# Optimization experiments

Hardware: AMD Instinct MI355X
Metric: run time of the kernel (lower is better)

## Reference

```python
import jax, jax.numpy as jnp
import numpy as np

N_ING, N_TASTE, D, E = 50000, 20000, 128, 600000


def setup_inputs() -> dict:
    key = jax.random.key(0)
    ks = jax.random.split(key, 13)
    s = 1.0 / np.sqrt(D)
    src = jax.random.randint(ks[2], (E,), 0, N_ING)
    dst = jax.random.randint(ks[3], (E,), 0, N_TASTE)
    return {
        "x_ing": jax.random.normal(ks[0], (N_ING, D), jnp.float32),
        "x_taste": jax.random.normal(ks[1], (N_TASTE, D), jnp.float32),
        "edge_index": jnp.stack([src, dst]),  # [2, E], row0=src(ingredient), row1=dst(taste)
        "W_ing": (jax.random.normal(ks[4], (D, D), jnp.float32) * s),
        "b_ing": jnp.zeros((D,), jnp.float32),
        "W_taste": (jax.random.normal(ks[5], (D, D), jnp.float32) * s),
        "b_taste": jnp.zeros((D,), jnp.float32),
        "a_src": (jax.random.normal(ks[6], (D,), jnp.float32) * s),
        "a_dst": (jax.random.normal(ks[7], (D,), jnp.float32) * s),
        "Wk": (jax.random.normal(ks[8], (D, D), jnp.float32) * s),
        "bk": jnp.zeros((D,), jnp.float32),
        "q": (jax.random.normal(ks[9], (D,), jnp.float32) * s),
    }


def reference(x_ing, x_taste, edge_index, W_ing, b_ing, W_taste, b_taste,
              a_src, a_dst, Wk, bk, q):
    # Input DictDropout(0.4) treated as identity (eval mode) for determinism.
    Nt = x_taste.shape[0]
    src, dst = edge_index[0], edge_index[1]

    # Per-node-type projections (HANConv.proj), heads=1 so head dim == D
    h_src = x_ing @ W_ing + b_ing      # [Ni, D]
    h_dst = x_taste @ W_taste + b_taste  # [Nt, D]

    # GAT-style additive attention logits
    al_src = h_src @ a_src  # [Ni]
    al_dst = h_dst @ a_dst  # [Nt]
    alpha = jax.nn.leaky_relu(al_src[src] + al_dst[dst], negative_slope=0.2)  # [E]

    # scatter-softmax over destination nodes
    amax = jax.ops.segment_max(alpha, dst, num_segments=Nt)        # [Nt]
    e = jnp.exp(alpha - amax[dst])                                  # [E]
    denom = jax.ops.segment_sum(e, dst, num_segments=Nt)           # [Nt]
    attn = e / jnp.maximum(denom[dst], 1e-16)                       # [E]

    # weighted scatter-add aggregation + ReLU (as in HANConv per edge type)
    msgs = h_src[src] * attn[:, None]                               # [E, D]
    out = jax.ops.segment_sum(msgs, dst, num_segments=Nt)          # [Nt, D]
    out = jax.nn.relu(out)

    # semantic attention across relation types (single relation -> beta == 1)
    score = jnp.sum(jnp.tanh(out @ Wk + bk).mean(axis=0) * q)       # scalar
    beta = jax.nn.softmax(score[None])[0]
    out = beta * out

    # TasteGNN applies GELU (torch default: exact erf form)
    return jax.nn.gelu(out, approximate=False)
```

## Files before the change

### kernel.cpp

```cpp
#include <hip/hip_runtime.h>
#include <hip/hip_bf16.h>

#define D 128
#define HB 288

using bf16x8 = __attribute__((ext_vector_type(8))) short;
using f32x4  = __attribute__((ext_vector_type(4))) float;

__device__ __forceinline__ ushort bf16bits(float f) {
    return __hip_bfloat16_raw(__float2bfloat16(f)).x;
}
__device__ __forceinline__ uint pack2(float lo, float hi) {
    return ((uint)bf16bits(hi) << 16) | (uint)bf16bits(lo);
}

__global__ __launch_bounds__(256)
void prep_kernel(const float* __restrict__ W_ing, const float* __restrict__ b_ing,
                 const float* __restrict__ W_taste, const float* __restrict__ b_taste,
                 const float* __restrict__ a_src, const float* __restrict__ a_dst,
                 ushort* __restrict__ Wt, float* __restrict__ v, float* __restrict__ consts,
                 int* __restrict__ count, int* __restrict__ total, int nt) {
    int t = threadIdx.x, b = blockIdx.x;
    if (b == 0) {
        __shared__ float red[D];
        int k = t;
        if (k < D) {
            float sv = 0.f;
            for (int d2 = 0; d2 < D; ++d2) sv += W_taste[k * D + d2] * a_dst[d2];
            v[k] = sv;
            red[k] = b_ing[k] * a_src[k];
        }
        __syncthreads();
        for (int s = 64; s > 0; s >>= 1) { if (k < s) red[k] += red[k + s]; __syncthreads(); }
        if (k == 0) consts[0] = red[0];
        __syncthreads();
        if (k < D) red[k] = b_taste[k] * a_dst[k];
        __syncthreads();
        for (int s = 64; s > 0; s >>= 1) { if (k < s) red[k] += red[k + s]; __syncthreads(); }
        if (k == 0) consts[1] = red[0];
    } else if (b <= 2) {
        int base = (b - 1) * 8192 + t * 32;
        #pragma unroll 8
        for (int i = 0; i < 32; ++i) {
            int idx = base + i;
            int n = idx >> 7, k = idx & 127;
            Wt[n * D + k] = bf16bits(W_ing[k * D + n]);
        }
    } else {
        int gid = (b - 3) * 256 + t;
        if (gid < nt) count[gid] = 0;
        if (gid == nt) *total = 0;
    }
}

__global__ __launch_bounds__(256)
void front_kernel(const float* __restrict__ x, const ushort* __restrict__ Wt,
                  const float* __restrict__ b, const float* __restrict__ avec,
                  const float* __restrict__ consts,
                  ushort* __restrict__ h16, float* __restrict__ al, int nrows, int GB,
                  const float* __restrict__ x_taste, const float* __restrict__ v,
                  int nt, float* __restrict__ al_dst,
                  const int* __restrict__ dstv, int E, int* __restrict__ count,
                  int* __restrict__ rank) {
    __shared__ __align__(16) ushort Xs[128 * 64];
    __shared__ __align__(16) ushort Ws[128 * 64];
    int t = threadIdx.x;

    if (blockIdx.x >= GB) {
        int rb = blockIdx.x - GB;
        if (rb < 512) {
            int lane = t & 63;
            int wave = rb * 4 + (t >> 6);
            float2 uv = ((const float2*)v)[lane];
            float c = consts[1];
            for (int r = wave; r < nt; r += 2048) {
                float2 xv = ((const float2*)(x_taste + (size_t)r * D))[lane];
                float p = xv.x * uv.x + xv.y * uv.y;
                #pragma unroll
                for (int off = 32; off; off >>= 1) p += __shfl_xor(p, off, 64);
                if (lane == 0) al_dst[r] = p + c;
            }
        } else {
            int tbase = (rb - 512) * 256 + t;
            int stride = HB * 256;
            for (int i0 = tbase; i0 < E; i0 += stride * 8) {
                int dv[8], idx[8], rv[8];
                #pragma unroll
                for (int k = 0; k < 8; ++k) {
                    idx[k] = i0 + k * stride;
                    dv[k] = (idx[k] < E) ? dstv[idx[k]] : -1;
                }
                #pragma unroll
                for (int k = 0; k < 8; ++k)
                    rv[k] = (dv[k] >= 0) ? atomicAdd(&count[dv[k]], 1) : 0;
                #pragma unroll
                for (int k = 0; k < 8; ++k)
                    if (dv[k] >= 0) rank[idx[k]] = rv[k];
            }
        }
        return;
    }

    int row0 = blockIdx.x * 128;
    int l = t & 63, w = t >> 6;
    int lr = l & 15, lq = l >> 4;
    f32x4 acc[2][8];
    #pragma unroll
    for (int i = 0; i < 2; ++i)
        #pragma unroll
        for (int j = 0; j < 8; ++j) acc[i][j] = f32x4{0.f, 0.f, 0.f, 0.f};

    int rowA0 = w * 32 + lr;
    int rowA1 = rowA0 + 16;
    int sw = lr & 7;
    int r = t >> 1;
    int kh = (t & 1) * 32;
    bool valid = (row0 + r) < nrows;

    #pragma unroll
    for (int h = 0; h < 2; ++h) {
        int k0 = h * 64;
        {
            const float* xp = x + (size_t)(row0 + r) * D + k0 + kh;
            const ushort* wp = Wt + (size_t)r * D + k0 + kh;
            int base_us = r * 64;
            #pragma unroll
            for (int j = 0; j < 4; ++j) {
                int c16 = (kh >> 3) + j;
                int off = base_us + ((c16 ^ (r & 7)) << 3);
                float4 a = valid ? *(const float4*)(xp + j * 8)     : make_float4(0.f, 0.f, 0.f, 0.f);
                float4 c = valid ? *(const float4*)(xp + j * 8 + 4) : make_float4(0.f, 0.f, 0.f, 0.f);
                uint4 pk;
                pk.x = pack2(a.x, a.y); pk.y = pack2(a.z, a.w);
                pk.z = pack2(c.x, c.y); pk.w = pack2(c.z, c.w);
                *(uint4*)&Xs[off] = pk;
                *(uint4*)&Ws[off] = *(const uint4*)(wp + j * 8);
            }
        }
        __syncthreads();
        #pragma unroll
        for (int s = 0; s < 2; ++s) {
            int c16 = s * 4 + lq;
            bf16x8 A0 = *(const bf16x8*)&Xs[rowA0 * 64 + ((c16 ^ sw) << 3)];
            bf16x8 A1 = *(const bf16x8*)&Xs[rowA1 * 64 + ((c16 ^ sw) << 3)];
            #pragma unroll
            for (int ct = 0; ct < 8; ++ct) {
                int rn = ct * 16 + lr;
                bf16x8 B = *(const bf16x8*)&Ws[rn * 64 + ((c16 ^ sw) << 3)];
                acc[0][ct] = __builtin_amdgcn_mfma_f32_16x16x32_bf16(A0, B, acc[0][ct], 0, 0, 0);
                acc[1][ct] = __builtin_amdgcn_mfma_f32_16x16x32_bf16(A1, B, acc[1][ct], 0, 0, 0);
            }
        }
        __syncthreads();
    }

    float bv[8], av[8];
    #pragma unroll
    for (int ct = 0; ct < 8; ++ct) { bv[ct] = b[ct * 16 + lr]; av[ct] = avec[ct * 16 + lr]; }
    float c0 = consts[0];
    #pragma unroll
    for (int rt = 0; rt < 2; ++rt) {
        #pragma unroll
        for (int rr = 0; rr < 4; ++rr) {
            int gr = row0 + w * 32 + rt * 16 + lq * 4 + rr;
            float p = 0.f;
            ushort hrow[8];
            #pragma unroll
            for (int ct = 0; ct < 8; ++ct) {
                float hv = acc[rt][ct][rr] + bv[ct];
                p = fmaf(hv, av[ct], p);
                hrow[ct] = bf16bits(hv);
            }
            p += __shfl_xor(p, 1, 64); p += __shfl_xor(p, 2, 64);
            p += __shfl_xor(p, 4, 64); p += __shfl_xor(p, 8, 64);
            if (gr < nrows) {
                #pragma unroll
                for (int ct = 0; ct < 8; ++ct)
                    h16[(size_t)gr * D + ct * 16 + lr] = hrow[ct];
                if (lr == 0) al[gr] = p + c0;
            }
        }
    }
}

__global__ __launch_bounds__(256)
void alloc_kernel(const int* __restrict__ count, int n, int* __restrict__ offs,
                  int* __restrict__ total) {
    int gid = blockIdx.x * blockDim.x + threadIdx.x;
    int lane = threadIdx.x & 63;
    int v = (gid < n) ? count[gid] : 0;
    int s = v;
    #pragma unroll
    for (int off = 1; off < 64; off <<= 1) {
        int t2 = __shfl_up(s, off, 64);
        if (lane >= off) s += t2;
    }
    int wavesum = __shfl(s, 63, 64);
    int base = 0;
    if (lane == 63) base = atomicAdd(total, wavesum);
    base = __shfl(base, 63, 64);
    if (gid < n) offs[gid] = base + s - v;
}

__global__ __launch_bounds__(256)
void scatter_kernel(const int* __restrict__ srcv, const int* __restrict__ dstv,
                    const int* __restrict__ rank, int E,
                    const int* __restrict__ offs, uint* __restrict__ es) {
    int tbase = blockIdx.x * blockDim.x + threadIdx.x;
    int stride = gridDim.x * blockDim.x;
    for (int i0 = tbase; i0 < E; i0 += stride * 4) {
        int idx[4], sv[4], dv[4], rv[4], ov[4];
        #pragma unroll
        for (int k = 0; k < 4; ++k) {
            idx[k] = i0 + k * stride;
            bool val = idx[k] < E;
            sv[k] = val ? srcv[idx[k]] : 0;
            dv[k] = val ? dstv[idx[k]] : 0;
            rv[k] = val ? rank[idx[k]] : 0;
        }
        #pragma unroll
        for (int k = 0; k < 4; ++k) ov[k] = offs[dv[k]];
        #pragma unroll
        for (int k = 0; k < 4; ++k)
            if (idx[k] < E) es[ov[k] + rv[k]] = (uint)sv[k];
    }
}

__global__ __launch_bounds__(256)
void agg_kernel(const ushort* __restrict__ h16, const int* __restrict__ offs,
                const int* __restrict__ count, const uint* __restrict__ es,
                const float* __restrict__ al_src, const float* __restrict__ al_dst,
                int nt, float* __restrict__ outp) {
    int lane = threadIdx.x & 63;
    int n = blockIdx.x * (blockDim.x >> 6) + (threadIdx.x >> 6);
    if (n >= nt) return;
    int beg = offs[n], cnt = count[n];
    float acc0 = 0.f, acc1 = 0.f;
    if (cnt > 0) {
        float ald = al_dst[n];
        uint s0 = 0, s1 = 0;
        float a0 = -1e30f, a1 = -1e30f;
        if (lane < cnt) {
            s0 = es[beg + lane];
            float t = al_src[s0] + ald; a0 = t > 0.f ? t : 0.2f * t;
        }
        if (64 + lane < cnt) {
            s1 = es[beg + 64 + lane];
            float t = al_src[s1] + ald; a1 = t > 0.f ? t : 0.2f * t;
        }
        float m = fmaxf(a0, a1);
        for (int i = 128 + lane; i < cnt; i += 64) {
            uint s = es[beg + i];
            float t = al_src[s] + ald; t = t > 0.f ? t : 0.2f * t;
            m = fmaxf(m, t);
        }
        #pragma unroll
        for (int off = 32; off; off >>= 1) m = fmaxf(m, __shfl_xor(m, off, 64));

        float w0 = (lane < cnt) ? __expf(a0 - m) : 0.f;
        float w1 = (64 + lane < cnt) ? __expf(a1 - m) : 0.f;
        float ssum = w0 + w1;
        for (int i = 128 + lane; i < cnt; i += 64) {
            uint s = es[beg + i];
            float t = al_src[s] + ald; t = t > 0.f ? t : 0.2f * t;
            ssum += __expf(t - m);
        }
        #pragma unroll
        for (int off = 32; off; off >>= 1) ssum += __shfl_xor(ssum, off, 64);
        float inv = 1.f / fmaxf(ssum, 1e-16f);

        for (int base = 0; base < cnt; base += 64) {
            uint pkl;
            if (base == 0)       pkl = (s0 << 16) | ((__float_as_uint(w0) + 0x8000u) >> 16);
            else if (base == 64) pkl = (s1 << 16) | ((__float_as_uint(w1) + 0x8000u) >> 16);
            else {
                pkl = 0;
                if (base + lane < cnt) {
                    uint s = es[beg + base + lane];
                    float t = al_src[s] + ald; t = t > 0.f ? t : 0.2f * t;
                    float wv = __expf(t - m);
                    pkl = (s << 16) | ((__float_as_uint(wv) + 0x8000u) >> 16);
                }
            }
            if (base + lane >= cnt) pkl = 0;
            int k = cnt - base; if (k > 64) k = 64;
            int kpad = (k + 7) & ~7;
            for (int i = 0; i < kpad; i += 8) {
                uint pk[8], hv[8];
                #pragma unroll
                for (int j = 0; j < 8; ++j) pk[j] = __shfl(pkl, i + j, 64);
                #pragma unroll
                for (int j = 0; j < 8; ++j) {
                    uint s2 = pk[j] >> 16;
                    hv[j] = ((const uint*)(h16 + (size_t)s2 * D))[lane];
                }
                #pragma unroll
                for (int j = 0; j < 8; ++j) {
                    float w  = __uint_as_float(pk[j] << 16);
                    float lo = __uint_as_float((hv[j] & 0xffffu) << 16);
                    float hi = __uint_as_float(hv[j] & 0xffff0000u);
                    acc0 = fmaf(w, lo, acc0);
                    acc1 = fmaf(w, hi, acc1);
                }
            }
        }
        acc0 *= inv; acc1 *= inv;
    }
    float o0 = acc0 > 0.f ? acc0 : 0.f;
    float o1 = acc1 > 0.f ? acc1 : 0.f;
    o0 = 0.5f * o0 * (1.f + erff(o0 * 0.70710678118654752f));
    o1 = 0.5f * o1 * (1.f + erff(o1 * 0.70710678118654752f));
    *(float2*)(outp + (size_t)n * D + 2 * lane) = make_float2(o0, o1);
}

extern "C" void kernel_launch(void* const* d_in, const int* in_sizes, int n_in,
                              void* d_out, int out_size, void* d_ws, size_t ws_size,
                              hipStream_t stream) {
    const float* x_ing   = (const float*)d_in[0];
    const float* x_taste = (const float*)d_in[1];
    const int*   edge    = (const int*)d_in[2];
    const float* W_ing   = (const float*)d_in[3];
    const float* b_ing   = (const float*)d_in[4];
    const float* W_taste = (const float*)d_in[5];
    const float* b_taste = (const float*)d_in[6];
    const float* a_src   = (const float*)d_in[7];
    const float* a_dst   = (const float*)d_in[8];
    float* outp = (float*)d_out;

    int Ni = in_sizes[0] / D;
    int Nt = in_sizes[1] / D;
    int E  = in_sizes[2] / 2;
    const int* srcv = edge;
    const int* dstv = edge + E;

    char* ws = (char*)d_ws;
    size_t off = 0;
    auto alloc = [&](size_t bytes) { void* p = ws + off; off += (bytes + 255) & ~(size_t)255; return p; };
    ushort* h16   = (ushort*)alloc((size_t)Ni * D * 2);
    ushort* Wt    = (ushort*)alloc((size_t)D * D * 2);
    float* v      = (float*)alloc(D * 4);
    float* consts = (float*)alloc(2 * 4);
    float* al_src = (float*)alloc((size_t)Ni * 4);
    float* al_dst = (float*)alloc((size_t)Nt * 4);
    int* count    = (int*)alloc((size_t)Nt * 4);
    int* offs     = (int*)alloc((size_t)Nt * 4);
    int* rank     = (int*)alloc((size_t)E * 4);
    int* total    = (int*)alloc(4);
    uint* es      = (uint*)alloc((size_t)E * 4);

    int GB = (Ni + 127) / 128;
    int zb = (Nt + 1 + 255) / 256;
    prep_kernel<<<3 + zb, 256, 0, stream>>>(W_ing, b_ing, W_taste, b_taste, a_src, a_dst,
                                            Wt, v, consts, count, total, Nt);
    front_kernel<<<GB + 512 + HB, 256, 0, stream>>>(x_ing, Wt, b_ing, a_src, consts,
                                                    h16, al_src, Ni, GB,
                                                    x_taste, v, Nt, al_dst,
                                                    dstv, E, count, rank);
    alloc_kernel<<<(Nt + 255) / 256, 256, 0, stream>>>(count, Nt, offs, total);
    int sb = (E + 256 * 4 - 1) / (256 * 4);
    scatter_kernel<<<sb, 256, 0, stream>>>(srcv, dstv, rank, E, offs, es);
    agg_kernel<<<(Nt + 3) / 4, 256, 0, stream>>>(h16, offs, count, es, al_src, al_dst, Nt, outp);
}
```

Measured before the change: 91.20 us.

## Replace global atomic counting sort with per-chunk LDS histograms and column scan

The edge-by-destination counting pass now builds a private shared-memory histogram per 8192-edge chunk instead of issuing global atomics on a shared count array. A new alloc kernel turns the per-chunk histograms into offsets by scanning across chunks for each destination, and the scatter kernel reads per-chunk offsets. This cuts contention on global atomics but adds an 80KB LDS union that can lower occupancy of the GEMM blocks, plus writes and reads of NB*Nt histogram entries. The shared-memory size is fixed at compile time to NT=20000.

```diff
diff --git a/kernel.cpp b/kernel.cpp
--- a/kernel.cpp
+++ b/kernel.cpp
@@ -2,7 +2,9 @@
 #include <hip/hip_bf16.h>
 
 #define D 128
-#define HB 288
+#define NT 20000
+#define CHUNK_SHIFT 13
+#define CHUNK (1 << CHUNK_SHIFT)
 
 using bf16x8 = __attribute__((ext_vector_type(8))) short;
 using f32x4  = __attribute__((ext_vector_type(4))) float;
@@ -19,7 +21,7 @@
                  const float* __restrict__ W_taste, const float* __restrict__ b_taste,
                  const float* __restrict__ a_src, const float* __restrict__ a_dst,
                  ushort* __restrict__ Wt, float* __restrict__ v, float* __restrict__ consts,
-                 int* __restrict__ count, int* __restrict__ total, int nt) {
+                 int* __restrict__ total) {
     int t = threadIdx.x, b = blockIdx.x;
     if (b == 0) {
         __shared__ float red[D];
@@ -47,9 +49,7 @@
             Wt[n * D + k] = bf16bits(W_ing[k * D + n]);
         }
     } else {
-        int gid = (b - 3) * 256 + t;
-        if (gid < nt) count[gid] = 0;
-        if (gid == nt) *total = 0;
+        if (t == 0) *total = 0;
     }
 }
 
@@ -60,10 +60,12 @@
                   ushort* __restrict__ h16, float* __restrict__ al, int nrows, int GB,
                   const float* __restrict__ x_taste, const float* __restrict__ v,
                   int nt, float* __restrict__ al_dst,
-                  const int* __restrict__ dstv, int E, int* __restrict__ count,
-                  int* __restrict__ rank) {
-    __shared__ __align__(16) ushort Xs[128 * 64];
-    __shared__ __align__(16) ushort Ws[128 * 64];
+                  const int* __restrict__ dstv, int E, int NB,
+                  int* __restrict__ hists, int* __restrict__ rank) {
+    __shared__ __align__(16) union {
+        struct { ushort Xs[128 * 64]; ushort Ws[128 * 64]; } g;
+        int hist[NT];
+    } sm;
     int t = threadIdx.x;
 
     if (blockIdx.x >= GB) {
@@ -81,22 +83,18 @@
                 if (lane == 0) al_dst[r] = p + c;
             }
         } else {
-            int tbase = (rb - 512) * 256 + t;
-            int stride = HB * 256;
-            for (int i0 = tbase; i0 < E; i0 += stride * 8) {
-                int dv[8], idx[8], rv[8];
-                #pragma unroll
-                for (int k = 0; k < 8; ++k) {
-                    idx[k] = i0 + k * stride;
-                    dv[k] = (idx[k] < E) ? dstv[idx[k]] : -1;
-                }
-                #pragma unroll
-                for (int k = 0; k < 8; ++k)
-                    rv[k] = (dv[k] >= 0) ? atomicAdd(&count[dv[k]], 1) : 0;
-                #pragma unroll
-                for (int k = 0; k < 8; ++k)
-                    if (dv[k] >= 0) rank[idx[k]] = rv[k];
-            }
+            int c = rb - 512;
+            for (int d = t; d < nt; d += 256) sm.hist[d] = 0;
+            __syncthreads();
+            int beg = c << CHUNK_SHIFT;
+            int end = beg + CHUNK; if (end > E) end = E;
+            for (int i = beg + t; i < end; i += 256) {
+                int d = dstv[i];
+                rank[i] = atomicAdd(&sm.hist[d], 1);
+            }
+            __syncthreads();
+            int* hb = hists + (size_t)c * nt;
+            for (int d = t; d < nt; d += 256) hb[d] = sm.hist[d];
         }
         return;
     }
@@ -133,20 +131,20 @@
                 uint4 pk;
                 pk.x = pack2(a.x, a.y); pk.y = pack2(a.z, a.w);
                 pk.z = pack2(c.x, c.y); pk.w = pack2(c.z, c.w);
-                *(uint4*)&Xs[off] = pk;
-                *(uint4*)&Ws[off] = *(const uint4*)(wp + j * 8);
+                *(uint4*)&sm.g.Xs[off] = pk;
+                *(uint4*)&sm.g.Ws[off] = *(const uint4*)(wp + j * 8);
             }
         }
         __syncthreads();
         #pragma unroll
         for (int s = 0; s < 2; ++s) {
             int c16 = s * 4 + lq;
-            bf16x8 A0 = *(const bf16x8*)&Xs[rowA0 * 64 + ((c16 ^ sw) << 3)];
-            bf16x8 A1 = *(const bf16x8*)&Xs[rowA1 * 64 + ((c16 ^ sw) << 3)];
+            bf16x8 A0 = *(const bf16x8*)&sm.g.Xs[rowA0 * 64 + ((c16 ^ sw) << 3)];
+            bf16x8 A1 = *(const bf16x8*)&sm.g.Xs[rowA1 * 64 + ((c16 ^ sw) << 3)];
             #pragma unroll
             for (int ct = 0; ct < 8; ++ct) {
                 int rn = ct * 16 + lr;
-                bf16x8 B = *(const bf16x8*)&Ws[rn * 64 + ((c16 ^ sw) << 3)];
+                bf16x8 B = *(const bf16x8*)&sm.g.Ws[rn * 64 + ((c16 ^ sw) << 3)];
                 acc[0][ct] = __builtin_amdgcn_mfma_f32_16x16x32_bf16(A0, B, acc[0][ct], 0, 0, 0);
                 acc[1][ct] = __builtin_amdgcn_mfma_f32_16x16x32_bf16(A1, B, acc[1][ct], 0, 0, 0);
             }
@@ -184,12 +182,20 @@
 }
 
 __global__ __launch_bounds__(256)
-void alloc_kernel(const int* __restrict__ count, int n, int* __restrict__ offs,
-                  int* __restrict__ total) {
+void alloc2_kernel(int* __restrict__ hists, int nt, int NB,
+                   int* __restrict__ offs, int* __restrict__ count,
+                   int* __restrict__ total) {
     int gid = blockIdx.x * blockDim.x + threadIdx.x;
     int lane = threadIdx.x & 63;
-    int v = (gid < n) ? count[gid] : 0;
-    int s = v;
+    int run = 0;
+    if (gid < nt) {
+        for (int b = 0; b < NB; ++b) {
+            int* p = &hists[(size_t)b * nt + gid];
+            int vv = *p; *p = run; run += vv;
+        }
+        count[gid] = run;
+    }
+    int s = run;
     #pragma unroll
     for (int off = 1; off < 64; off <<= 1) {
         int t2 = __shfl_up(s, off, 64);
@@ -199,13 +205,17 @@
     int base = 0;
     if (lane == 63) base = atomicAdd(total, wavesum);
     base = __shfl(base, 63, 64);
-    if (gid < n) offs[gid] = base + s - v;
+    if (gid < nt) {
+        int o = base + s - run;
+        offs[gid] = o;
+        for (int b = 0; b < NB; ++b) hists[(size_t)b * nt + gid] += o;
+    }
 }
 
 __global__ __launch_bounds__(256)
 void scatter_kernel(const int* __restrict__ srcv, const int* __restrict__ dstv,
-                    const int* __restrict__ rank, int E,
-                    const int* __restrict__ offs, uint* __restrict__ es) {
+                    const int* __restrict__ rank, int E, int nt,
+                    const int* __restrict__ hists, uint* __restrict__ es) {
     int tbase = blockIdx.x * blockDim.x + threadIdx.x;
     int stride = gridDim.x * blockDim.x;
     for (int i0 = tbase; i0 < E; i0 += stride * 4) {
@@ -219,7 +229,10 @@
             rv[k] = val ? rank[idx[k]] : 0;
         }
         #pragma unroll
-        for (int k = 0; k < 4; ++k) ov[k] = offs[dv[k]];
+        for (int k = 0; k < 4; ++k) {
+            int b = idx[k] >> CHUNK_SHIFT;
+            ov[k] = (idx[k] < E) ? hists[(size_t)b * nt + dv[k]] : 0;
+        }
         #pragma unroll
         for (int k = 0; k < 4; ++k)
             if (idx[k] < E) es[ov[k] + rv[k]] = (uint)sv[k];
@@ -347,17 +360,18 @@
     int* rank     = (int*)alloc((size_t)E * 4);
     int* total    = (int*)alloc(4);
     uint* es      = (uint*)alloc((size_t)E * 4);
+    int NB = (E + CHUNK - 1) >> CHUNK_SHIFT;
+    int* hists    = (int*)alloc((size_t)NB * Nt * 4);
 
     int GB = (Ni + 127) / 128;
-    int zb = (Nt + 1 + 255) / 256;
-    prep_kernel<<<3 + zb, 256, 0, stream>>>(W_ing, b_ing, W_taste, b_taste, a_src, a_dst,
-                                            Wt, v, consts, count, total, Nt);
-    front_kernel<<<GB + 512 + HB, 256, 0, stream>>>(x_ing, Wt, b_ing, a_src, consts,
+    prep_kernel<<<4, 256, 0, stream>>>(W_ing, b_ing, W_taste, b_taste, a_src, a_dst,
+                                       Wt, v, consts, total);
+    front_kernel<<<GB + 512 + NB, 256, 0, stream>>>(x_ing, Wt, b_ing, a_src, consts,
                                                     h16, al_src, Ni, GB,
                                                     x_taste, v, Nt, al_dst,
-                                                    dstv, E, count, rank);
-    alloc_kernel<<<(Nt + 255) / 256, 256, 0, stream>>>(count, Nt, offs, total);
+                                                    dstv, E, NB, hists, rank);
+    alloc2_kernel<<<(Nt + 255) / 256, 256, 0, stream>>>(hists, Nt, NB, offs, count, total);
     int sb = (E + 256 * 4 - 1) / (256 * 4);
-    scatter_kernel<<<sb, 256, 0, stream>>>(srcv, dstv, rank, E, offs, es);
+    scatter_kernel<<<sb, 256, 0, stream>>>(srcv, dstv, rank, E, Nt, hists, es);
     agg_kernel<<<(Nt + 3) / 4, 256, 0, stream>>>(h16, offs, count, es, al_src, al_dst, Nt, outp);
 }
```

Result: slower. 106.8 us (+17.1%).
